# Performance work log

Measured on AMD Instinct MI355X. Metric: run time of the kernel, lower is better.

Reference implementation:

```python
import jax, jax.numpy as jnp
import numpy as np

B, T, C = 256, 1024, 128
D = C // 2          # split_len1 == split_len2 == 64
CLAMP = 5.0


def setup_inputs() -> dict:
    key = jax.random.key(0)
    ks = jax.random.split(key, 13)
    p = lambda k, s: jax.random.normal(k, s, dtype=jnp.float32) * 0.1
    inp = {"x": jax.random.normal(ks[0], (B, T, C), dtype=jnp.float32)}
    for i, name in enumerate(["s1", "s2"]):
        b = 1 + i * 6
        inp[name + "_Wx"] = p(ks[b], (D, 3 * D))
        inp[name + "_Wh"] = p(ks[b + 1], (D, 3 * D))
        inp[name + "_bx"] = p(ks[b + 2], (3 * D,))
        inp[name + "_bh"] = p(ks[b + 3], (3 * D,))
        inp[name + "_Wo"] = p(ks[b + 4], (D, 2 * D))
        inp[name + "_bo"] = p(ks[b + 5], (2 * D,))
    return inp


def _gru(x, h, Wx, Wh, bx, bh, Wo, bo):
    # GRU cell with hidden size == input size, plus output projection (F_GRU).
    gx = x @ Wx + bx
    gh = h @ Wh + bh
    rx, zx, nx = jnp.split(gx, 3, axis=-1)
    rh, zh, nh = jnp.split(gh, 3, axis=-1)
    r = jax.nn.sigmoid(rx + rh)
    z = jax.nn.sigmoid(zx + zh)
    n = jnp.tanh(nx + r * nh)
    h_next = (1.0 - z) * n + z * h
    return h_next @ Wo + bo, h_next


def _e(s):
    # exp(clamp * 0.636 * atan(s / clamp)) -- soft-clamped scale
    return jnp.exp(CLAMP * 0.636 * jnp.arctan(s / CLAMP))


def reference(x, s1_Wx, s1_Wh, s1_bx, s1_bh, s1_Wo, s1_bo,
              s2_Wx, s2_Wh, s2_bx, s2_bh, s2_Wo, s2_bo):
    def step(carry, x_t):
        h1, h2 = carry
        x1, x2 = x_t[:, :D], x_t[:, D:]
        r2, h2n = _gru(x2, h2, s2_Wx, s2_Wh, s2_bx, s2_bh, s2_Wo, s2_bo)
        s2v, t2 = r2[:, :D], r2[:, D:]
        y1 = _e(s2v) * x1 + t2
        r1, h1n = _gru(y1, h1, s1_Wx, s1_Wh, s1_bx, s1_bh, s1_Wo, s1_bo)
        s1v, t1 = r1[:, :D], r1[:, D:]
        y2 = _e(s1v) * x2 + t1
        return (h1n, h2n), jnp.concatenate([y1, y2], axis=-1)

    h0 = (jnp.zeros((x.shape[0], D), x.dtype), jnp.zeros((x.shape[0], D), x.dtype))
    _, ys = jax.lax.scan(step, h0, jnp.swapaxes(x, 0, 1))  # scan over T
    return jnp.swapaxes(ys, 0, 1)  # [B, T, C]
```

## Files before the change

kernel.cpp:

```cpp
#include <hip/hip_runtime.h>

#define NB 256
#define NT 1024
#define NC 128
#define ND 64
#define SP 16
#define NSL 32
#define NJ 68
#define PXW 196
#define PHW 72

typedef _Float16 f16x8 __attribute__((ext_vector_type(8)));
typedef float f32x4 __attribute__((ext_vector_type(4)));
typedef _Float16 f16x2_t __attribute__((ext_vector_type(2)));

__device__ __forceinline__ float fexp2(float x){
#if __has_builtin(__builtin_amdgcn_exp2f)
  return __builtin_amdgcn_exp2f(x);
#else
  return exp2f(x);
#endif
}
__device__ __forceinline__ float frcp_(float x){
#if __has_builtin(__builtin_amdgcn_rcpf)
  return __builtin_amdgcn_rcpf(x);
#else
  return 1.0f / x;
#endif
}
__device__ __forceinline__ float sigmoid_f(float x){
  return frcp_(1.0f + fexp2(-1.4426950408889634f * x));
}
__device__ __forceinline__ float tanh_f(float x){
  return 1.0f - 2.0f * frcp_(fexp2(2.8853900817779268f * x) + 1.0f);
}
__device__ __forceinline__ float e_func(float s){
  float u = 0.2f * s;
  float au = fabsf(u);
  bool inv = au > 1.0f;
  float v = inv ? frcp_(au) : au;
  float v2 = v * v;
  float pp = -0.0117212f;
  pp = pp * v2 + 0.05265332f;
  pp = pp * v2 - 0.11643287f;
  pp = pp * v2 + 0.19354346f;
  pp = pp * v2 - 0.33262347f;
  pp = pp * v2 + 0.99997726f;
  float at = pp * v;
  if (inv) at = 1.5707963267948966f - at;
  at = __builtin_copysignf(at, u);
  return fexp2(4.5877702301963f * at);
}

#define BAR() asm volatile("s_waitcnt lgkmcnt(0)\n\ts_barrier" ::: "memory")

__device__ __forceinline__ f16x8 bld(const float* __restrict__ W, int ldw,
                                     int ks, int tile, int lane){
  f16x8 v;
  const int kb = ks*32 + 8*(lane>>4);
  const int c  = tile*16 + (lane&15);
  #pragma unroll
  for (int j = 0; j < 8; ++j) v[j] = (_Float16)W[(kb + j)*ldw + c];
  return v;
}
__device__ __forceinline__ f16x8 ldafb(const _Float16* ring, int t0, int lane, int ks){
  return *reinterpret_cast<const f16x8*>(
      reinterpret_cast<const char*>(ring)
      + (((t0 & (NSL-1)) + (lane & 15)) * (PHW*2)) + 16*(lane>>4) + 64*ks);
}
#define MFMA16(acc, a, bfr) acc = __builtin_amdgcn_mfma_f32_16x16x32_f16(a, bfr, acc, 0, 0, 0)

__device__ __forceinline__ float fdot2u(unsigned a, unsigned b, float c){
#if __has_builtin(__builtin_amdgcn_fdot2)
  return __builtin_amdgcn_fdot2(__builtin_bit_cast(f16x2_t, a), __builtin_bit_cast(f16x2_t, b), c, false);
#else
  f16x2_t av = __builtin_bit_cast(f16x2_t, a);
  f16x2_t bv = __builtin_bit_cast(f16x2_t, b);
  return c + (float)av[0]*(float)bv[0] + (float)av[1]*(float)bv[1];
#endif
}
__device__ __forceinline__ unsigned packh(float a, float b){
  union { _Float16 h[2]; unsigned u; } v;
  v.h[0] = (_Float16)a; v.h[1] = (_Float16)b;
  return v.u;
}
__device__ __forceinline__ float dpp_xor1(float v){
  int r = __builtin_amdgcn_update_dpp(0, __builtin_bit_cast(int, v),
                                      0xB1, 0xF, 0xF, true);
  return __builtin_bit_cast(float, r);
}
__device__ __forceinline__ f16x8 packx8(float4 u, float4 v){
  f16x8 r;
  r[0]=(_Float16)u.x; r[1]=(_Float16)u.y; r[2]=(_Float16)u.z; r[3]=(_Float16)u.w;
  r[4]=(_Float16)v.x; r[5]=(_Float16)v.y; r[6]=(_Float16)v.z; r[7]=(_Float16)v.w;
  return r;
}

__global__ __launch_bounds__(384, 1)
void glow_gru_kernel(const float* __restrict__ x,
                     const float* __restrict__ Wx1, const float* __restrict__ Wh1,
                     const float* __restrict__ bx1, const float* __restrict__ bh1,
                     const float* __restrict__ Wo1, const float* __restrict__ bo1,
                     const float* __restrict__ Wx2, const float* __restrict__ Wh2,
                     const float* __restrict__ bx2, const float* __restrict__ bh2,
                     const float* __restrict__ Wo2, const float* __restrict__ bo2,
                     float* __restrict__ out)
{
  __shared__ __align__(16) _Float16 h2p[NSL][PHW];
  __shared__ __align__(16) _Float16 y1p[NSL][PHW];
  __shared__ __align__(16) _Float16 h1p[NSL][PHW];
  __shared__ float px2[NSL][PXW];
  __shared__ float py1[NSL][PXW];

  const int l = threadIdx.x;
  const int w = l >> 6;
  const int i = l & 63;
  const int b = blockIdx.x;
  const long xbase = (long)b * NT * NC;

  if (w == 0){
    f16x8 bf[12][2];
    #pragma unroll
    for (int t = 0; t < 12; ++t){ bf[t][0] = bld(Wx2,192,0,t,i); bf[t][1] = bld(Wx2,192,1,t,i); }
    const float* pxA = x + xbase + 64 + (long)(i & 15)*NC + 8*(i >> 4);
    __syncthreads();
    for (int J = 0; J <= NJ; ++J){
      const int t0 = SP*J;
      if (t0 < NT){
        const float* base = pxA + (long)t0*NC;
        float4 u0 = *(const float4*)(base);
        float4 u1 = *(const float4*)(base + 4);
        float4 v0 = *(const float4*)(base + 32);
        float4 v1 = *(const float4*)(base + 36);
        f16x8 a0 = packx8(u0, u1);
        f16x8 a1 = packx8(v0, v1);
        f32x4 zz = {0.f,0.f,0.f,0.f};
        f32x4 acc[12];
        #pragma unroll
        for (int t2 = 0; t2 < 12; ++t2){
          acc[t2] = zz;
          MFMA16(acc[t2], a0, bf[t2][0]);
          MFMA16(acc[t2], a1, bf[t2][1]);
        }
        const int rb = (t0 + 4*(i>>4)) & (NSL-1);
        #pragma unroll
        for (int t2 = 0; t2 < 12; ++t2){
          #pragma unroll
          for (int rg = 0; rg < 4; ++rg)
            px2[rb + rg][t2*16 + (i&15)] = acc[t2][rg];
        }
      }
      BAR();
    }
  } else if (w == 1){
    f16x8 bf[12][2];
    #pragma unroll
    for (int t = 0; t < 12; ++t){ bf[t][0] = bld(Wx1,192,0,t,i); bf[t][1] = bld(Wx1,192,1,t,i); }
    __syncthreads();
    for (int J = 0; J <= NJ; ++J){
      const int t0 = SP*(J-3);
      if (t0 >= 0 && t0 < NT){
        f16x8 a0 = ldafb(&y1p[0][0], t0, i, 0);
        f16x8 a1 = ldafb(&y1p[0][0], t0, i, 1);
        f32x4 zz = {0.f,0.f,0.f,0.f};
        f32x4 acc[12];
        #pragma unroll
        for (int t2 = 0; t2 < 12; ++t2){
          acc[t2] = zz;
          MFMA16(acc[t2], a0, bf[t2][0]);
          MFMA16(acc[t2], a1, bf[t2][1]);
        }
        const int rb = (t0 + 4*(i>>4)) & (NSL-1);
        #pragma unroll
        for (int t2 = 0; t2 < 12; ++t2){
          #pragma unroll
          for (int rg = 0; rg < 4; ++rg)
            py1[rb + rg][t2*16 + (i&15)] = acc[t2][rg];
        }
      }
      BAR();
    }
  } else if (w == 2 || w == 3){
    const bool isA = (w == 2);
    const float* WH = isA ? Wh2 : Wh1;
    const float* bx = isA ? bx2 : bx1;
    const float* bh = isA ? bh2 : bh1;
    _Float16 (*hr)[PHW] = isA ? h2p : h1p;
    float (*pr)[PXW]    = isA ? px2 : py1;
    const int lag = isA ? 1 : 4;
    unsigned wr[32], wz[32], wn[32];
    #pragma unroll
    for (int k2 = 0; k2 < 32; ++k2){
      wr[k2] = packh(WH[(2*k2)*192 + i],       WH[(2*k2+1)*192 + i]);
      wz[k2] = packh(WH[(2*k2)*192 + 64 + i],  WH[(2*k2+1)*192 + 64 + i]);
      wn[k2] = packh(WH[(2*k2)*192 + 128 + i], WH[(2*k2+1)*192 + 128 + i]);
    }
    int addrs[32];
    #pragma unroll
    for (int q = 0; q < 32; ++q) addrs[q] = 8*q;
    const float b0 = bx[i] + bh[i];
    const float b1 = bx[64+i] + bh[64+i];
    const float b2v = bx[128+i], b3v = bh[128+i];
    float h = 0.f;
    __syncthreads();
    for (int J = 0; J <= NJ; ++J){
      const int t0 = SP*(J - lag);
      if (t0 >= 0 && t0 < NT){
        #pragma unroll
        for (int s = 0; s < SP; ++s){
          const int t = t0 + s;
          float hsw = dpp_xor1(h);
          float lo = (i & 1) ? hsw : h;
          float hp = (i & 1) ? h : hsw;
          int pk = __builtin_bit_cast(int, __builtin_amdgcn_cvt_pkrtz(lo, hp));
          int hv[32];
          #pragma unroll
          for (int q = 0; q < 32; ++q) hv[q] = __builtin_amdgcn_ds_bpermute(addrs[q], pk);
          float rx = pr[t&(NSL-1)][i];
          float zx = pr[t&(NSL-1)][64+i];
          float nx = pr[t&(NSL-1)][128+i];
          float rh0=0.f, rh1=0.f, zh0=0.f, zh1=0.f, nh0=0.f, nh1=0.f;
          #pragma unroll
          for (int k2 = 0; k2 < 16; ++k2){
            rh0 = fdot2u((unsigned)hv[k2],    wr[k2],    rh0);
            zh0 = fdot2u((unsigned)hv[k2],    wz[k2],    zh0);
            nh0 = fdot2u((unsigned)hv[k2],    wn[k2],    nh0);
            rh1 = fdot2u((unsigned)hv[16+k2], wr[16+k2], rh1);
            zh1 = fdot2u((unsigned)hv[16+k2], wz[16+k2], zh1);
            nh1 = fdot2u((unsigned)hv[16+k2], wn[16+k2], nh1);
          }
          float r = sigmoid_f(rx + rh0 + rh1 + b0);
          float z = sigmoid_f(zx + zh0 + zh1 + b1);
          float nn = tanh_f(nx + b2v + r*(nh0 + nh1 + b3v));
          h = (1.f - z)*nn + z*h;
          hr[t&(NSL-1)][i] = (_Float16)h;
        }
      }
      BAR();
    }
  } else {
    const bool isB = (w == 4);
    const float* WO = isB ? Wo2 : Wo1;
    const float* bo = isB ? bo2 : bo1;
    _Float16 (*hr)[PHW] = isB ? h2p : h1p;
    const int lag  = isB ? 2 : 5;
    const int xoff = isB ? 0 : 64;
    f16x8 bf[8][2];
    #pragma unroll
    for (int t = 0; t < 8; ++t){ bf[t][0] = bld(WO,128,0,t,i); bf[t][1] = bld(WO,128,1,t,i); }
    const int c = i & 15;
    float bS[4], bT[4];
    #pragma unroll
    for (int t2 = 0; t2 < 4; ++t2){
      bS[t2] = bo[t2*16 + c];
      bT[t2] = bo[64 + t2*16 + c];
    }
    float xg[4][4], xn[4][4];
    __syncthreads();
    for (int J = 0; J <= NJ; ++J){
      const int t0 = SP*(J - lag);
      const int t0n = t0 + SP;
      if (t0n >= 0 && t0n < NT){
        #pragma unroll
        for (int t2 = 0; t2 < 4; ++t2){
          #pragma unroll
          for (int rg = 0; rg < 4; ++rg){
            const int t = t0n + 4*(i>>4) + rg;
            xn[t2][rg] = x[xbase + (long)t*NC + xoff + t2*16 + c];
          }
        }
      }
      if (t0 == 0){
        #pragma unroll
        for (int t2 = 0; t2 < 4; ++t2){
          #pragma unroll
          for (int rg = 0; rg < 4; ++rg){
            const int t = t0 + 4*(i>>4) + rg;
            xg[t2][rg] = x[xbase + (long)t*NC + xoff + t2*16 + c];
          }
        }
      }
      if (t0 >= 0 && t0 < NT){
        f16x8 a0 = ldafb(&hr[0][0], t0, i, 0);
        f16x8 a1 = ldafb(&hr[0][0], t0, i, 1);
        f32x4 zz = {0.f,0.f,0.f,0.f};
        f32x4 acc[8];
        #pragma unroll
        for (int t2 = 0; t2 < 8; ++t2){
          acc[t2] = zz;
          MFMA16(acc[t2], a0, bf[t2][0]);
          MFMA16(acc[t2], a1, bf[t2][1]);
        }
        #pragma unroll
        for (int t2 = 0; t2 < 4; ++t2){
          #pragma unroll
          for (int rg = 0; rg < 4; ++rg){
            const int t = t0 + 4*(i>>4) + rg;
            float y = e_func(acc[t2][rg] + bS[t2]) * xg[t2][rg] + (acc[t2+4][rg] + bT[t2]);
            out[xbase + (long)t*NC + xoff + t2*16 + c] = y;
            if (isB) y1p[t & (NSL-1)][t2*16 + c] = (_Float16)y;
          }
        }
      }
      #pragma unroll
      for (int t2 = 0; t2 < 4; ++t2)
        #pragma unroll
        for (int rg = 0; rg < 4; ++rg) xg[t2][rg] = xn[t2][rg];
      BAR();
    }
  }
}

extern "C" void kernel_launch(void* const* d_in, const int* in_sizes, int n_in,
                              void* d_out, int out_size, void* d_ws, size_t ws_size,
                              hipStream_t stream) {
  const float* x   = (const float*)d_in[0];
  const float* Wx1 = (const float*)d_in[1];
  const float* Wh1 = (const float*)d_in[2];
  const float* bx1 = (const float*)d_in[3];
  const float* bh1 = (const float*)d_in[4];
  const float* Wo1 = (const float*)d_in[5];
  const float* bo1 = (const float*)d_in[6];
  const float* Wx2 = (const float*)d_in[7];
  const float* Wh2 = (const float*)d_in[8];
  const float* bx2 = (const float*)d_in[9];
  const float* bh2 = (const float*)d_in[10];
  const float* Wo2 = (const float*)d_in[11];
  const float* bo2 = (const float*)d_in[12];
  float* out = (float*)d_out;

  hipLaunchKernelGGL(glow_gru_kernel, dim3(NB), dim3(384), 0, stream,
                     x, Wx1, Wh1, bx1, bh1, Wo1, bo1,
                     Wx2, Wh2, bx2, bh2, Wo2, bo2, out);
}
```

Measured before the change: 355.3 us.

## Broadcast GRU hidden state via readlane and prefetch gate inputs per block

In the recurrent GRU warps, the 32 ds_bpermute ops that broadcast packed fp16 hidden pairs are replaced with v_readlane scalar reads. Since every lane needs the same values, this moves the broadcast off the LDS crossbar into SGPRs. The per-step LDS loads of the x-side gate preactivations for all 16 steps are hoisted ahead of the serial loop, and wave priority is raised during the recurrence. The aim is to shorten the latency-bound critical path of the serial hidden-state update, at the cost of more registers and readlane-to-VALU dependency stalls.

```diff
diff --git a/kernel.cpp b/kernel.cpp
--- a/kernel.cpp
+++ b/kernel.cpp
@@ -195,9 +195,6 @@
       wz[k2] = packh(WH[(2*k2)*192 + 64 + i],  WH[(2*k2+1)*192 + 64 + i]);
       wn[k2] = packh(WH[(2*k2)*192 + 128 + i], WH[(2*k2+1)*192 + 128 + i]);
     }
-    int addrs[32];
-    #pragma unroll
-    for (int q = 0; q < 32; ++q) addrs[q] = 8*q;
     const float b0 = bx[i] + bh[i];
     const float b1 = bx[64+i] + bh[64+i];
     const float b2v = bx[128+i], b3v = bh[128+i];
@@ -206,6 +203,14 @@
     for (int J = 0; J <= NJ; ++J){
       const int t0 = SP*(J - lag);
       if (t0 >= 0 && t0 < NT){
+        float rxs[SP], zxs[SP], nxs[SP];
+        #pragma unroll
+        for (int s = 0; s < SP; ++s){
+          rxs[s] = pr[(t0+s)&(NSL-1)][i];
+          zxs[s] = pr[(t0+s)&(NSL-1)][64+i];
+          nxs[s] = pr[(t0+s)&(NSL-1)][128+i];
+        }
+        __builtin_amdgcn_s_setprio(1);
         #pragma unroll
         for (int s = 0; s < SP; ++s){
           const int t = t0 + s;
@@ -213,28 +218,27 @@
           float lo = (i & 1) ? hsw : h;
           float hp = (i & 1) ? h : hsw;
           int pk = __builtin_bit_cast(int, __builtin_amdgcn_cvt_pkrtz(lo, hp));
-          int hv[32];
-          #pragma unroll
-          for (int q = 0; q < 32; ++q) hv[q] = __builtin_amdgcn_ds_bpermute(addrs[q], pk);
-          float rx = pr[t&(NSL-1)][i];
-          float zx = pr[t&(NSL-1)][64+i];
-          float nx = pr[t&(NSL-1)][128+i];
+          unsigned hv[32];
+          #pragma unroll
+          for (int q = 0; q < 32; ++q)
+            hv[q] = (unsigned)__builtin_amdgcn_readlane(pk, 2*q);
           float rh0=0.f, rh1=0.f, zh0=0.f, zh1=0.f, nh0=0.f, nh1=0.f;
           #pragma unroll
           for (int k2 = 0; k2 < 16; ++k2){
-            rh0 = fdot2u((unsigned)hv[k2],    wr[k2],    rh0);
-            zh0 = fdot2u((unsigned)hv[k2],    wz[k2],    zh0);
-            nh0 = fdot2u((unsigned)hv[k2],    wn[k2],    nh0);
-            rh1 = fdot2u((unsigned)hv[16+k2], wr[16+k2], rh1);
-            zh1 = fdot2u((unsigned)hv[16+k2], wz[16+k2], zh1);
-            nh1 = fdot2u((unsigned)hv[16+k2], wn[16+k2], nh1);
+            rh0 = fdot2u(hv[k2],    wr[k2],    rh0);
+            zh0 = fdot2u(hv[k2],    wz[k2],    zh0);
+            nh0 = fdot2u(hv[k2],    wn[k2],    nh0);
+            rh1 = fdot2u(hv[16+k2], wr[16+k2], rh1);
+            zh1 = fdot2u(hv[16+k2], wz[16+k2], zh1);
+            nh1 = fdot2u(hv[16+k2], wn[16+k2], nh1);
           }
-          float r = sigmoid_f(rx + rh0 + rh1 + b0);
-          float z = sigmoid_f(zx + zh0 + zh1 + b1);
-          float nn = tanh_f(nx + b2v + r*(nh0 + nh1 + b3v));
+          float r = sigmoid_f(rxs[s] + rh0 + rh1 + b0);
+          float z = sigmoid_f(zxs[s] + zh0 + zh1 + b1);
+          float nn = tanh_f(nxs[s] + b2v + r*(nh0 + nh1 + b3v));
           h = (1.f - z)*nn + z*h;
           hr[t&(NSL-1)][i] = (_Float16)h;
         }
+        __builtin_amdgcn_s_setprio(0);
       }
       BAR();
     }
```

New measurement: 357.9 us. Within noise of the previous version (+0.7%).
